# Kernel optimization log

Measured on AMD Instinct MI355X. Metric: run time of the kernel, lower is better.

The kernel has to match this reference:

```python
import jax, jax.numpy as jnp
import numpy as np

THRESHOLD = 0.05
TOP_N = 512
NMS_THR = 0.6
POST_TOP_N = 100
MIN_SIZE = 0.0
N_CLASS = 8
IMG_SIZE = (256.0, 256.0, 64.0)
B, C, H, W, D = 4, 8, 128, 128, 32


def _pairwise_iou3d(b):
    # b: [K, 6] in xyzxyz; returns [K, K] volumetric IoU
    lo, hi = b[:, :3], b[:, 3:]
    ilo = jnp.maximum(lo[:, None, :], lo[None, :, :])
    ihi = jnp.minimum(hi[:, None, :], hi[None, :, :])
    inter = jnp.prod(jnp.maximum(ihi - ilo, 0.0), axis=-1)
    vol = jnp.prod(jnp.maximum(hi - lo, 0.0), axis=-1)
    return inter / (vol[:, None] + vol[None, :] - inter + 1e-9)


def _nms_keep(boxes, scores, thr):
    # greedy NMS; scores == -1 marks invalid entries. Returns bool keep mask [K].
    K = boxes.shape[0]
    order = jnp.argsort(-scores)
    b = boxes[order]
    s = scores[order]
    iou = _pairwise_iou3d(b)
    idx = jnp.arange(K)

    def body(i, keep):
        sup = (iou[i] > thr) & keep[i] & (idx > i)
        return keep & ~sup

    keep = jax.lax.fori_loop(0, K, body, s > 0.0)
    return jnp.zeros(K, dtype=bool).at[order].set(keep)


def _forward(location, cls_pred, box_pred, center_pred):
    Bb, Cc = cls_pred.shape[0], cls_pred.shape[1]
    N = cls_pred.shape[2] * cls_pred.shape[3] * cls_pred.shape[4]
    # [B, C, H, W, D] -> [B, N, C]
    cls = jax.nn.sigmoid(cls_pred).transpose(0, 2, 3, 4, 1).reshape(Bb, N, Cc)
    ctr = jax.nn.sigmoid(center_pred).transpose(0, 2, 3, 4, 1).reshape(Bb, N)
    box = box_pred.transpose(0, 2, 3, 4, 1).reshape(Bb, N, 6)

    candid = cls > THRESHOLD                      # [B, N, C]
    scores = cls * ctr[:, :, None]                # centerness-weighted
    flat = jnp.where(candid, scores, -1.0).reshape(Bb, N * Cc)
    vals, idx = jax.lax.top_k(flat, TOP_N)        # fixed-size stand-in for mask+topk
    valid = vals > 0.0                            # matches torch clamp(count, top_n)

    loc_idx = idx // Cc                           # flattened spatial location
    class_id = idx % Cc + 1                       # labels are 1-based
    bsel = jnp.take_along_axis(box, loc_idx[..., None], axis=1)   # [B, K, 6]
    lsel = location[loc_idx]                                      # [B, K, 3]
    det = jnp.concatenate([lsel - bsel[..., :3], lsel + bsel[..., 3:]], axis=-1)

    # BoxList.clip to image volume
    full = jnp.concatenate([jnp.asarray(IMG_SIZE), jnp.asarray(IMG_SIZE)]).astype(det.dtype) - 1.0
    det = jnp.clip(det, 0.0, full)

    score = jnp.where(valid, jnp.sqrt(jnp.where(valid, vals, 1.0)), 0.0)

    # remove_small_boxes
    sides = det[..., 3:] - det[..., :3]
    valid = valid & jnp.all(sides >= MIN_SIZE, axis=-1)

    # per-class greedy NMS (decisions are non-differentiable; torch detaches anyway)
    det_ng = jax.lax.stop_gradient(det)
    score_ng = jax.lax.stop_gradient(score)

    def per_image(b_i, s_i, c_i, v_i):
        def per_class(j):
            m = v_i & (c_i == j)
            return _nms_keep(b_i, jnp.where(m, s_i, -1.0), NMS_THR) & m
        return jnp.any(jax.vmap(per_class)(jnp.arange(1, N_CLASS + 1)), axis=0)

    valid = jax.vmap(per_image)(det_ng, score_ng, class_id, valid)

    # post_top_n selection (kthvalue threshold == keep top post_top_n scores)
    fv, fi = jax.lax.top_k(jnp.where(valid, score_ng, -1.0), POST_TOP_N)
    fvalid = fv > 0.0
    fbox = jnp.take_along_axis(det, fi[..., None], axis=1) * fvalid[..., None]
    fscore = jnp.where(fvalid, jnp.take_along_axis(score, fi, axis=1), 0.0)
    flabel = jnp.where(fvalid, jnp.take_along_axis(class_id, fi, axis=1), 0)
    return fbox, fscore, flabel, fvalid


def setup_inputs() -> dict:
    key = jax.random.key(0)
    k1, k2, k3, k4 = jax.random.split(key, 4)
    N = H * W * D
    location = jax.random.uniform(k1, (N, 3), dtype=jnp.float32) * jnp.asarray(IMG_SIZE, jnp.float32)
    cls_pred = jax.random.normal(k2, (B, C, H, W, D), dtype=jnp.float32) - 2.0  # realistic logits
    box_pred = jax.random.uniform(k3, (B, 6, H, W, D), dtype=jnp.float32) * 20.0  # positive extents
    center_pred = jax.random.normal(k4, (B, 1, H, W, D), dtype=jnp.float32)
    return {"location": location, "cls_pred": cls_pred, "box_pred": box_pred, "center_pred": center_pred}


def reference(location, cls_pred, box_pred, center_pred):
    return _forward(location, cls_pred, box_pred, center_pred)
```

## Files before the change

### kernel.cpp

```cpp
#include <hip/hip_runtime.h>

#define NB 4
#define NC 8
#define NLOC 524288
#define TOPN 512
#define POST 100
#define NBIN 8192
#define SELBINS 4096
#define SCAP 4096
#define CAP 16384
#define KPT 16
#define LCAP 2048
#define NMS_THR 0.6f
#define CAND_THR 0.05f
#define SPEC_THR 0.5f

typedef unsigned long long ull;

#define OFF_CNT    0
#define OFF_OVF    16
#define OFF_KEYS   64
#define ZERO_BYTES 32

__device__ __forceinline__ float sigmoidf_(float x) {
    return 1.0f / (1.0f + __expf(-x));
}

__global__ __launch_bounds__(256) void gather_spec(const float* __restrict__ cls,
                                                   const float* __restrict__ ctr,
                                                   ull* __restrict__ keys,
                                                   unsigned int* __restrict__ counts,
                                                   unsigned int* __restrict__ ovf) {
    __shared__ ull lkeys[LCAP];
    __shared__ unsigned int lcnt;
    __shared__ unsigned int lbase;
    const int b = blockIdx.y;
    if (threadIdx.x == 0) lcnt = 0;
    __syncthreads();

    const int n0 = (blockIdx.x * blockDim.x + threadIdx.x) * 8;
    const float4* cvp = (const float4*)(ctr + (size_t)b * NLOC + n0);
    const float4 cv0 = cvp[0], cv1 = cvp[1];
    float4 cl0[NC], cl1[NC];
    #pragma unroll
    for (int c = 0; c < NC; ++c) {
        const float4* p = (const float4*)(cls + ((size_t)b * NC + c) * NLOC + n0);
        cl0[c] = p[0];
        cl1[c] = p[1];
    }

    #pragma unroll
    for (int h = 0; h < 2; ++h) {
        const float4 cv = h ? cv1 : cv0;
        #pragma unroll
        for (int j = 0; j < 4; ++j) {
            bool any = false;
            #pragma unroll
            for (int c = 0; c < NC; ++c) {
                const float x = h ? ((const float*)&cl1[c])[j] : ((const float*)&cl0[c])[j];
                any |= (x > 0.0f);
            }
            if (any) {
                const float sc = sigmoidf_(((const float*)&cv)[j]);
                #pragma unroll
                for (int c = 0; c < NC; ++c) {
                    const float x = h ? ((const float*)&cl1[c])[j] : ((const float*)&cl0[c])[j];
                    if (x > 0.0f) {
                        const float p = sigmoidf_(x) * sc;
                        if (p > SPEC_THR) {
                            const unsigned pos = atomicAdd(&lcnt, 1u);
                            if (pos < LCAP) {
                                const unsigned flat = (unsigned)((n0 + h * 4 + j) * NC + c);
                                lkeys[pos] = ((ull)__float_as_uint(p) << 32) | (unsigned)(~flat);
                            }
                        }
                    }
                }
            }
        }
    }
    __syncthreads();
    const unsigned m = lcnt;
    if (threadIdx.x == 0) {
        const unsigned stored = (m > LCAP) ? LCAP : m;
        lbase = atomicAdd(&counts[b], stored);
        if (m > LCAP) ovf[b] = 1;
    }
    __syncthreads();
    const unsigned stored = (m > LCAP) ? LCAP : m;
    const unsigned base = lbase;
    for (unsigned i = threadIdx.x; i < stored; i += blockDim.x) {
        const unsigned pos = base + i;
        if (pos < CAP) keys[(size_t)b * CAP + pos] = lkeys[i];
    }
}

__device__ __forceinline__ float iou3d_(const float* a, const float* bx) {
    const float ix = fminf(a[3], bx[3]) - fmaxf(a[0], bx[0]);
    const float iy = fminf(a[4], bx[4]) - fmaxf(a[1], bx[1]);
    const float iz = fminf(a[5], bx[5]) - fmaxf(a[2], bx[2]);
    const float inter = fmaxf(ix, 0.0f) * fmaxf(iy, 0.0f) * fmaxf(iz, 0.0f);
    const float v0 = fmaxf(a[3] - a[0], 0.0f) * fmaxf(a[4] - a[1], 0.0f) * fmaxf(a[5] - a[2], 0.0f);
    const float v1 = fmaxf(bx[3] - bx[0], 0.0f) * fmaxf(bx[4] - bx[1], 0.0f) * fmaxf(bx[5] - bx[2], 0.0f);
    return inter / (v0 + v1 - inter + 1e-9f);
}

__global__ __launch_bounds__(1024) void select_nms_kernel(const float* __restrict__ cls,
                                                          const float* __restrict__ ctr,
                                                          ull* __restrict__ keys,
                                                          unsigned int* __restrict__ counts,
                                                          const unsigned int* __restrict__ ovf,
                                                          const float* __restrict__ loc,
                                                          const float* __restrict__ box,
                                                          float* __restrict__ out) {
    __shared__ union SU {
        struct { unsigned int hist[SELBINS]; ull surv[SCAP]; } sel;
        unsigned int fhist[NBIN];
        struct { float sd[TOPN * 6]; float ss[TOPN]; int scl[TOPN];
                 int keep[TOPN]; int clist[NC][TOPN]; int wcnt[NC]; } nms;
    } u;
    __shared__ ull tk[TOPN];
    __shared__ unsigned int scnt;
    __shared__ int cut_s;

    const int b = blockIdx.x, t = threadIdx.x;

    {
        const unsigned cnt0 = counts[b];
        const bool bad = !(cnt0 >= TOPN && cnt0 <= CAP && ovf[b] == 0);
        if (bad) {
            for (int i = t; i < NBIN; i += 1024) u.fhist[i] = 0;
            __syncthreads();
            for (int n = t; n < NLOC; n += 1024) {
                const float sc = sigmoidf_(ctr[(size_t)b * NLOC + n]);
                #pragma unroll
                for (int c = 0; c < NC; ++c) {
                    const float s = sigmoidf_(cls[((size_t)b * NC + c) * NLOC + n]);
                    if (s > CAND_THR) atomicAdd(&u.fhist[__float_as_uint(s * sc) >> 17], 1u);
                }
            }
            __syncthreads();
            if (t == 0) {
                unsigned cum = 0; int bin = 0;
                for (int i = NBIN - 1; i >= 0; --i) {
                    cum += u.fhist[i];
                    if (cum >= TOPN) { bin = i; break; }
                }
                cut_s = bin;
                counts[b] = 0;
            }
            __syncthreads();
            const unsigned cb2 = (unsigned)cut_s;
            for (int n = t; n < NLOC; n += 1024) {
                const float sc = sigmoidf_(ctr[(size_t)b * NLOC + n]);
                #pragma unroll
                for (int c = 0; c < NC; ++c) {
                    const float s = sigmoidf_(cls[((size_t)b * NC + c) * NLOC + n]);
                    if (s > CAND_THR) {
                        const unsigned bits = __float_as_uint(s * sc);
                        if ((bits >> 17) >= cb2) {
                            const unsigned pos = atomicAdd(&counts[b], 1u);
                            if (pos < CAP)
                                keys[(size_t)b * CAP + pos] =
                                    ((ull)bits << 32) | (unsigned)(~(unsigned)(n * NC + c));
                        }
                    }
                }
            }
            __threadfence();
        }
    }
    __syncthreads();

    const int M = (int)min(counts[b], (unsigned)CAP);

    ull kr[KPT];
    {
        const ulonglong2* kb = (const ulonglong2*)(keys + (size_t)b * CAP);
        #pragma unroll
        for (int p = 0; p < KPT / 2; ++p) {
            const ulonglong2 v = kb[p * 1024 + t];
            kr[2 * p] = v.x;
            kr[2 * p + 1] = v.y;
        }
    }

    for (int i = t; i < SELBINS; i += 1024) u.sel.hist[i] = 0;
    if (t == 0) scnt = 0;
    if (t < TOPN) tk[t] = 0;
    __syncthreads();
    #pragma unroll
    for (int p = 0; p < KPT / 2; ++p) {
        #pragma unroll
        for (int q = 0; q < 2; ++q) {
            const int i = 2 * (p * 1024 + t) + q;
            if (i < M) {
                const unsigned hi = (unsigned)(kr[2 * p + q] >> 32);
                const int off = (int)hi - 0x3F000000;
                int bin = (off < 0) ? 0 : (off >> 11);
                if (bin > SELBINS - 1) bin = SELBINS - 1;
                atomicAdd(&u.sel.hist[bin], 1u);
            }
        }
    }
    __syncthreads();

    if (t < 64) {
        unsigned s = 0;
        for (int i = 0; i < 64; ++i)
            s += u.sel.hist[t * 64 + ((i + t) & 63)];
        unsigned suf = s;
        #pragma unroll
        for (int d = 1; d < 64; d <<= 1) {
            const unsigned o = __shfl_down(suf, d);
            suf += (t + d < 64) ? o : 0u;
        }
        const ull mask = __ballot(suf >= TOPN);
        unsigned nxt = __shfl_down(suf, 1);
        if (t == 63) nxt = 0;
        if (mask == 0ull) {
            if (t == 0) cut_s = 0;
        } else {
            const int L = 63 - __builtin_clzll(mask);
            if (t == L) {
                unsigned cum = nxt;
                int c = L * 64;
                for (int i = 63; i >= 0; --i) {
                    cum += u.sel.hist[L * 64 + i];
                    if (cum >= TOPN) { c = L * 64 + i; break; }
                }
                cut_s = c;
            }
        }
    }
    __syncthreads();

    const int cb = cut_s;
    #pragma unroll
    for (int p = 0; p < KPT / 2; ++p) {
        #pragma unroll
        for (int q = 0; q < 2; ++q) {
            const int i = 2 * (p * 1024 + t) + q;
            if (i < M) {
                const ull k = kr[2 * p + q];
                const unsigned hi = (unsigned)(k >> 32);
                const int off = (int)hi - 0x3F000000;
                int bin = (off < 0) ? 0 : (off >> 11);
                if (bin > SELBINS - 1) bin = SELBINS - 1;
                if (bin >= cb) {
                    const unsigned p2 = atomicAdd(&scnt, 1u);
                    if (p2 < SCAP) u.sel.surv[p2] = k;
                }
            }
        }
    }
    __syncthreads();

    const unsigned sc_final = scnt;
    if (sc_final <= (unsigned)SCAP) {
        const int S = (int)sc_final;
        for (int i = t; i < S; i += 1024) {
            const ull ke = u.sel.surv[i];
            int r = 0;
            for (int j = 0; j < S; ++j) r += (u.sel.surv[j] > ke) ? 1 : 0;
            if (r < TOPN) tk[r] = ke;
        }
    } else {
        for (int i = t; i < M; i += 1024) {
            const ull ke = keys[(size_t)b * CAP + i];
            int r = 0;
            for (int j = 0; j < M; ++j) r += (keys[(size_t)b * CAP + j] > ke) ? 1 : 0;
            if (r < TOPN) tk[r] = ke;
        }
    }
    __syncthreads();

    if (t < TOPN) {
        const ull k = tk[t];
        const unsigned bits = (unsigned)(k >> 32);
        const float val = __uint_as_float(bits);
        int valid = (val > 0.0f) ? 1 : 0;
        const unsigned flat = ~(unsigned)(k & 0xffffffffu);
        int n = 0, c = 0;
        if (valid) { n = (int)(flat >> 3); c = (int)(flat & 7u); }
        const float lx = loc[n * 3 + 0], ly = loc[n * 3 + 1], lz = loc[n * 3 + 2];
        const float* bp = box + (size_t)b * 6 * NLOC + n;
        const float b0 = bp[0];
        const float b1 = bp[(size_t)NLOC];
        const float b2 = bp[2 * (size_t)NLOC];
        const float b3 = bp[3 * (size_t)NLOC];
        const float b4 = bp[4 * (size_t)NLOC];
        const float b5 = bp[5 * (size_t)NLOC];
        const float d0 = fminf(fmaxf(lx - b0, 0.0f), 255.0f);
        const float d1 = fminf(fmaxf(ly - b1, 0.0f), 255.0f);
        const float d2 = fminf(fmaxf(lz - b2, 0.0f), 63.0f);
        const float d3 = fminf(fmaxf(lx + b3, 0.0f), 255.0f);
        const float d4 = fminf(fmaxf(ly + b4, 0.0f), 255.0f);
        const float d5 = fminf(fmaxf(lz + b5, 0.0f), 63.0f);
        if (d3 - d0 < 0.0f || d4 - d1 < 0.0f || d5 - d2 < 0.0f) valid = 0;
        u.nms.sd[t * 6 + 0] = d0; u.nms.sd[t * 6 + 1] = d1; u.nms.sd[t * 6 + 2] = d2;
        u.nms.sd[t * 6 + 3] = d3; u.nms.sd[t * 6 + 4] = d4; u.nms.sd[t * 6 + 5] = d5;
        u.nms.ss[t] = (val > 0.0f) ? sqrtf(val) : 0.0f;
        u.nms.scl[t] = c + 1;
        u.nms.keep[t] = valid;
    }
    __syncthreads();

    if (t < TOPN) {
        const int w = t >> 6, lane = t & 63;
        const int myclass = w + 1;
        int cnt = 0;
        for (int j0 = 0; j0 < TOPN; j0 += 64) {
            const int j = j0 + lane;
            const bool pred = (u.nms.scl[j] == myclass) && (u.nms.keep[j] != 0);
            const ull m = __ballot(pred);
            if (pred) {
                const int pos = cnt + __popcll(m & ((1ull << lane) - 1ull));
                u.nms.clist[w][pos] = j;
            }
            cnt += __popcll(m);
        }
        __threadfence_block();

        if (cnt <= 128) {
            const int g0 = (lane < cnt) ? u.nms.clist[w][lane] : -1;
            const int g1 = (lane + 64 < cnt) ? u.nms.clist[w][lane + 64] : -1;
            float B0[6], B1[6];
            #pragma unroll
            for (int q = 0; q < 6; ++q) {
                B0[q] = (g0 >= 0) ? u.nms.sd[g0 * 6 + q] : 0.0f;
                B1[q] = (g1 >= 0) ? u.nms.sd[g1 * 6 + q] : 0.0f;
            }
            bool a0 = (g0 >= 0), a1 = (g1 >= 0);
            ull m0 = __ballot(a0), m1 = __ballot(a1);
            for (int i = 0; i < cnt; ++i) {
                const int ki = i >> 6, li = i & 63;
                const ull mi = ki ? m1 : m0;
                if (!((mi >> li) & 1ull)) continue;
                float pb[6];
                #pragma unroll
                for (int q = 0; q < 6; ++q) pb[q] = __shfl(ki ? B1[q] : B0[q], li);
                if (a0 && lane > i)      { if (iou3d_(B0, pb) > NMS_THR) a0 = false; }
                if (a1 && lane + 64 > i) { if (iou3d_(B1, pb) > NMS_THR) a1 = false; }
                m0 = __ballot(a0); m1 = __ballot(a1);
            }
            if (g0 >= 0 && !a0) u.nms.keep[g0] = 0;
            if (g1 >= 0 && !a1) u.nms.keep[g1] = 0;
        } else {
            volatile int* vkeep = u.nms.keep;
            const float* sd = u.nms.sd;
            for (int i = 0; i < cnt; ++i) {
                const int gi = u.nms.clist[w][i];
                if (!vkeep[gi]) continue;
                float pb[6];
                #pragma unroll
                for (int q = 0; q < 6; ++q) pb[q] = sd[gi * 6 + q];
                for (int e = i + 1 + lane; e < cnt; e += 64) {
                    const int gj = u.nms.clist[w][e];
                    if (vkeep[gj]) {
                        float cb_[6];
                        #pragma unroll
                        for (int q = 0; q < 6; ++q) cb_[q] = sd[gj * 6 + q];
                        if (iou3d_(cb_, pb) > NMS_THR) vkeep[gj] = 0;
                    }
                }
                __threadfence_block();
            }
        }
    }
    __syncthreads();

    if (t < TOPN) {
        const int w = t >> 6, lane = t & 63;
        const ull km = __ballot(u.nms.keep[t] != 0);
        if (lane == 0) u.nms.wcnt[w] = __popcll(km);
    }
    __syncthreads();
    if (t < TOPN) {
        const int w = t >> 6, lane = t & 63;
        const ull km = __ballot(u.nms.keep[t] != 0);
        int before = 0, total = 0;
        #pragma unroll
        for (int w2 = 0; w2 < NC; ++w2) {
            total += u.nms.wcnt[w2];
            if (w2 < w) before += u.nms.wcnt[w2];
        }
        const int myrank = before + __popcll(km & ((1ull << lane) - 1ull));

        float* fbox = out;
        float* fscore = out + NB * POST * 6;
        float* flabel = out + NB * POST * 7;
        float* fvalid = out + NB * POST * 8;

        if (u.nms.keep[t] && myrank < POST) {
            #pragma unroll
            for (int k = 0; k < 6; ++k) fbox[(b * POST + myrank) * 6 + k] = u.nms.sd[t * 6 + k];
            fscore[b * POST + myrank] = u.nms.ss[t];
            flabel[b * POST + myrank] = (float)u.nms.scl[t];
            fvalid[b * POST + myrank] = 1.0f;
        }
        const int tc = (total < POST) ? total : POST;
        if (t >= tc && t < POST) {
            #pragma unroll
            for (int k = 0; k < 6; ++k) fbox[(b * POST + t) * 6 + k] = 0.0f;
            fscore[b * POST + t] = 0.0f;
            flabel[b * POST + t] = 0.0f;
            fvalid[b * POST + t] = 0.0f;
        }
    }
}

extern "C" void kernel_launch(void* const* d_in, const int* in_sizes, int n_in,
                              void* d_out, int out_size, void* d_ws, size_t ws_size,
                              hipStream_t stream) {
    const float* location = (const float*)d_in[0];
    const float* cls_pred = (const float*)d_in[1];
    const float* box_pred = (const float*)d_in[2];
    const float* ctr_pred = (const float*)d_in[3];

    char* ws = (char*)d_ws;
    unsigned int* counts = (unsigned int*)(ws + OFF_CNT);
    unsigned int* ovf    = (unsigned int*)(ws + OFF_OVF);
    ull*          keys   = (ull*)(ws + OFF_KEYS);

    hipMemsetAsync(d_ws, 0, ZERO_BYTES, stream);

    gather_spec<<<dim3(NLOC / 2048, NB), 256, 0, stream>>>(cls_pred, ctr_pred, keys, counts, ovf);
    select_nms_kernel<<<NB, 1024, 0, stream>>>(cls_pred, ctr_pred, keys, counts, ovf,
                                               location, box_pred, (float*)d_out);
}
```

Baseline: 85.96 us.

## Split select/NMS into separate kernels and precompute IoU suppression bitmasks

The monolithic select+NMS kernel is split into three kernels: top-k selection writing to a global buffer, a decode kernel spread over more blocks to gather boxes, and an NMS/output kernel. Within NMS, pairwise IoU suppression bits are computed up front into per-lane bitmasks, so the serial greedy loop only does bit tests and ballots instead of shuffles and IoU math. Key loads are also guarded by count, and the rank-count loops are unrolled. This adds two kernel launches, a larger memset, and global round-trips through workspace.

```diff
diff --git a/kernel.cpp b/kernel.cpp
--- a/kernel.cpp
+++ b/kernel.cpp
@@ -19,8 +19,13 @@
 
 #define OFF_CNT    0
 #define OFF_OVF    16
-#define OFF_KEYS   64
-#define ZERO_BYTES 32
+#define OFF_TOPK   64
+#define OFF_DET    16448
+#define OFF_SS     65600
+#define OFF_SCL    73792
+#define OFF_KEEP   81984
+#define OFF_KEYS   90176
+#define ZERO_BYTES 16448
 
 __device__ __forceinline__ float sigmoidf_(float x) {
     return 1.0f / (1.0f + __expf(-x));
@@ -105,21 +110,16 @@
     return inter / (v0 + v1 - inter + 1e-9f);
 }
 
-__global__ __launch_bounds__(1024) void select_nms_kernel(const float* __restrict__ cls,
-                                                          const float* __restrict__ ctr,
-                                                          ull* __restrict__ keys,
-                                                          unsigned int* __restrict__ counts,
-                                                          const unsigned int* __restrict__ ovf,
-                                                          const float* __restrict__ loc,
-                                                          const float* __restrict__ box,
-                                                          float* __restrict__ out) {
+__global__ __launch_bounds__(1024) void select_kernel(const float* __restrict__ cls,
+                                                      const float* __restrict__ ctr,
+                                                      ull* __restrict__ keys,
+                                                      unsigned int* __restrict__ counts,
+                                                      const unsigned int* __restrict__ ovf,
+                                                      ull* __restrict__ tk_g) {
     __shared__ union SU {
         struct { unsigned int hist[SELBINS]; ull surv[SCAP]; } sel;
         unsigned int fhist[NBIN];
-        struct { float sd[TOPN * 6]; float ss[TOPN]; int scl[TOPN];
-                 int keep[TOPN]; int clist[NC][TOPN]; int wcnt[NC]; } nms;
     } u;
-    __shared__ ull tk[TOPN];
     __shared__ unsigned int scnt;
     __shared__ int cut_s;
 
@@ -179,7 +179,9 @@
         const ulonglong2* kb = (const ulonglong2*)(keys + (size_t)b * CAP);
         #pragma unroll
         for (int p = 0; p < KPT / 2; ++p) {
-            const ulonglong2 v = kb[p * 1024 + t];
+            const int vi = p * 1024 + t;
+            ulonglong2 v; v.x = 0; v.y = 0;
+            if (2 * vi < M) v = kb[vi];
             kr[2 * p] = v.x;
             kr[2 * p + 1] = v.y;
         }
@@ -187,7 +189,6 @@
 
     for (int i = t; i < SELBINS; i += 1024) u.sel.hist[i] = 0;
     if (t == 0) scnt = 0;
-    if (t < TOPN) tk[t] = 0;
     __syncthreads();
     #pragma unroll
     for (int p = 0; p < KPT / 2; ++p) {
@@ -207,6 +208,7 @@
 
     if (t < 64) {
         unsigned s = 0;
+        #pragma unroll 8
         for (int i = 0; i < 64; ++i)
             s += u.sel.hist[t * 64 + ((i + t) & 63)];
         unsigned suf = s;
@@ -262,141 +264,181 @@
         for (int i = t; i < S; i += 1024) {
             const ull ke = u.sel.surv[i];
             int r = 0;
-            for (int j = 0; j < S; ++j) r += (u.sel.surv[j] > ke) ? 1 : 0;
-            if (r < TOPN) tk[r] = ke;
+            int j = 0;
+            for (; j + 16 <= S; j += 16) {
+                #pragma unroll
+                for (int q = 0; q < 16; ++q) r += (u.sel.surv[j + q] > ke) ? 1 : 0;
+            }
+            for (; j < S; ++j) r += (u.sel.surv[j] > ke) ? 1 : 0;
+            if (r < TOPN) tk_g[b * TOPN + r] = ke;
         }
     } else {
         for (int i = t; i < M; i += 1024) {
             const ull ke = keys[(size_t)b * CAP + i];
             int r = 0;
             for (int j = 0; j < M; ++j) r += (keys[(size_t)b * CAP + j] > ke) ? 1 : 0;
-            if (r < TOPN) tk[r] = ke;
-        }
-    }
-    __syncthreads();
-
-    if (t < TOPN) {
-        const ull k = tk[t];
-        const unsigned bits = (unsigned)(k >> 32);
-        const float val = __uint_as_float(bits);
-        int valid = (val > 0.0f) ? 1 : 0;
-        const unsigned flat = ~(unsigned)(k & 0xffffffffu);
-        int n = 0, c = 0;
-        if (valid) { n = (int)(flat >> 3); c = (int)(flat & 7u); }
-        const float lx = loc[n * 3 + 0], ly = loc[n * 3 + 1], lz = loc[n * 3 + 2];
-        const float* bp = box + (size_t)b * 6 * NLOC + n;
-        const float b0 = bp[0];
-        const float b1 = bp[(size_t)NLOC];
-        const float b2 = bp[2 * (size_t)NLOC];
-        const float b3 = bp[3 * (size_t)NLOC];
-        const float b4 = bp[4 * (size_t)NLOC];
-        const float b5 = bp[5 * (size_t)NLOC];
-        const float d0 = fminf(fmaxf(lx - b0, 0.0f), 255.0f);
-        const float d1 = fminf(fmaxf(ly - b1, 0.0f), 255.0f);
-        const float d2 = fminf(fmaxf(lz - b2, 0.0f), 63.0f);
-        const float d3 = fminf(fmaxf(lx + b3, 0.0f), 255.0f);
-        const float d4 = fminf(fmaxf(ly + b4, 0.0f), 255.0f);
-        const float d5 = fminf(fmaxf(lz + b5, 0.0f), 63.0f);
-        if (d3 - d0 < 0.0f || d4 - d1 < 0.0f || d5 - d2 < 0.0f) valid = 0;
-        u.nms.sd[t * 6 + 0] = d0; u.nms.sd[t * 6 + 1] = d1; u.nms.sd[t * 6 + 2] = d2;
-        u.nms.sd[t * 6 + 3] = d3; u.nms.sd[t * 6 + 4] = d4; u.nms.sd[t * 6 + 5] = d5;
-        u.nms.ss[t] = (val > 0.0f) ? sqrtf(val) : 0.0f;
-        u.nms.scl[t] = c + 1;
-        u.nms.keep[t] = valid;
-    }
-    __syncthreads();
-
-    if (t < TOPN) {
-        const int w = t >> 6, lane = t & 63;
-        const int myclass = w + 1;
-        int cnt = 0;
-        for (int j0 = 0; j0 < TOPN; j0 += 64) {
-            const int j = j0 + lane;
-            const bool pred = (u.nms.scl[j] == myclass) && (u.nms.keep[j] != 0);
-            const ull m = __ballot(pred);
-            if (pred) {
-                const int pos = cnt + __popcll(m & ((1ull << lane) - 1ull));
-                u.nms.clist[w][pos] = j;
-            }
-            cnt += __popcll(m);
-        }
-        __threadfence_block();
-
-        if (cnt <= 128) {
-            const int g0 = (lane < cnt) ? u.nms.clist[w][lane] : -1;
-            const int g1 = (lane + 64 < cnt) ? u.nms.clist[w][lane + 64] : -1;
-            float B0[6], B1[6];
+            if (r < TOPN) tk_g[b * TOPN + r] = ke;
+        }
+    }
+}
+
+__global__ __launch_bounds__(64) void decode_kernel(const ull* __restrict__ tk_g,
+                                                    const float* __restrict__ loc,
+                                                    const float* __restrict__ box,
+                                                    float* __restrict__ det,
+                                                    float* __restrict__ ss,
+                                                    int* __restrict__ scl,
+                                                    int* __restrict__ keepo) {
+    const int b = blockIdx.y;
+    const int t = blockIdx.x * 64 + threadIdx.x;
+    const ull k = tk_g[b * TOPN + t];
+    const unsigned bits = (unsigned)(k >> 32);
+    const float val = __uint_as_float(bits);
+    int valid = (val > 0.0f) ? 1 : 0;
+    const unsigned flat = ~(unsigned)(k & 0xffffffffu);
+    int n = 0, c = 0;
+    if (valid) { n = (int)(flat >> 3); c = (int)(flat & 7u); }
+    const float lx = loc[n * 3 + 0], ly = loc[n * 3 + 1], lz = loc[n * 3 + 2];
+    const float* bp = box + (size_t)b * 6 * NLOC + n;
+    const float b0 = bp[0];
+    const float b1 = bp[(size_t)NLOC];
+    const float b2 = bp[2 * (size_t)NLOC];
+    const float b3 = bp[3 * (size_t)NLOC];
+    const float b4 = bp[4 * (size_t)NLOC];
+    const float b5 = bp[5 * (size_t)NLOC];
+    const float d0 = fminf(fmaxf(lx - b0, 0.0f), 255.0f);
+    const float d1 = fminf(fmaxf(ly - b1, 0.0f), 255.0f);
+    const float d2 = fminf(fmaxf(lz - b2, 0.0f), 63.0f);
+    const float d3 = fminf(fmaxf(lx + b3, 0.0f), 255.0f);
+    const float d4 = fminf(fmaxf(ly + b4, 0.0f), 255.0f);
+    const float d5 = fminf(fmaxf(lz + b5, 0.0f), 63.0f);
+    if (d3 - d0 < 0.0f || d4 - d1 < 0.0f || d5 - d2 < 0.0f) valid = 0;
+    const int o = b * TOPN + t;
+    det[o * 6 + 0] = d0; det[o * 6 + 1] = d1; det[o * 6 + 2] = d2;
+    det[o * 6 + 3] = d3; det[o * 6 + 4] = d4; det[o * 6 + 5] = d5;
+    ss[o] = (val > 0.0f) ? sqrtf(val) : 0.0f;
+    scl[o] = c + 1;
+    keepo[o] = valid;
+}
+
+__global__ __launch_bounds__(512) void nms_out_kernel(const float* __restrict__ det,
+                                                      const float* __restrict__ score,
+                                                      const int* __restrict__ clsid,
+                                                      const int* __restrict__ validin,
+                                                      float* __restrict__ out) {
+    __shared__ float sd[TOPN * 6];
+    __shared__ float ss[TOPN];
+    __shared__ int scl[TOPN];
+    __shared__ int keep[TOPN];
+    __shared__ int clist[NC][TOPN];
+    __shared__ int wcnt[NC];
+    const int b = blockIdx.x, t = threadIdx.x;
+    const int w = t >> 6, lane = t & 63;
+
+    {
+        const float* dp = det + (size_t)(b * TOPN) * 6;
+        for (int i = t; i < TOPN * 6; i += 512) sd[i] = dp[i];
+    }
+    ss[t] = score[b * TOPN + t];
+    scl[t] = clsid[b * TOPN + t];
+    keep[t] = validin[b * TOPN + t];
+    __syncthreads();
+
+    const int myclass = w + 1;
+    int cnt = 0;
+    for (int j0 = 0; j0 < TOPN; j0 += 64) {
+        const int j = j0 + lane;
+        const bool pred = (scl[j] == myclass) && (keep[j] != 0);
+        const ull m = __ballot(pred);
+        if (pred) {
+            const int pos = cnt + __popcll(m & ((1ull << lane) - 1ull));
+            clist[w][pos] = j;
+        }
+        cnt += __popcll(m);
+    }
+    __threadfence_block();
+
+    if (cnt <= 128) {
+        const int g0 = (lane < cnt) ? clist[w][lane] : -1;
+        const int g1 = (lane + 64 < cnt) ? clist[w][lane + 64] : -1;
+        float A0[6], A1[6];
+        #pragma unroll
+        for (int q = 0; q < 6; ++q) {
+            A0[q] = (g0 >= 0) ? sd[g0 * 6 + q] : 0.0f;
+            A1[q] = (g1 >= 0) ? sd[g1 * 6 + q] : 0.0f;
+        }
+        ull s0 = 0, s1lo = 0, s1hi = 0;
+        for (int i = 0; i < cnt; ++i) {
+            const int gi = clist[w][i];
+            float pb[6];
             #pragma unroll
-            for (int q = 0; q < 6; ++q) {
-                B0[q] = (g0 >= 0) ? u.nms.sd[g0 * 6 + q] : 0.0f;
-                B1[q] = (g1 >= 0) ? u.nms.sd[g1 * 6 + q] : 0.0f;
-            }
-            bool a0 = (g0 >= 0), a1 = (g1 >= 0);
-            ull m0 = __ballot(a0), m1 = __ballot(a1);
-            for (int i = 0; i < cnt; ++i) {
-                const int ki = i >> 6, li = i & 63;
-                const ull mi = ki ? m1 : m0;
-                if (!((mi >> li) & 1ull)) continue;
-                float pb[6];
-                #pragma unroll
-                for (int q = 0; q < 6; ++q) pb[q] = __shfl(ki ? B1[q] : B0[q], li);
-                if (a0 && lane > i)      { if (iou3d_(B0, pb) > NMS_THR) a0 = false; }
-                if (a1 && lane + 64 > i) { if (iou3d_(B1, pb) > NMS_THR) a1 = false; }
-                m0 = __ballot(a0); m1 = __ballot(a1);
-            }
-            if (g0 >= 0 && !a0) u.nms.keep[g0] = 0;
-            if (g1 >= 0 && !a1) u.nms.keep[g1] = 0;
-        } else {
-            volatile int* vkeep = u.nms.keep;
-            const float* sd = u.nms.sd;
-            for (int i = 0; i < cnt; ++i) {
-                const int gi = u.nms.clist[w][i];
-                if (!vkeep[gi]) continue;
-                float pb[6];
-                #pragma unroll
-                for (int q = 0; q < 6; ++q) pb[q] = sd[gi * 6 + q];
-                for (int e = i + 1 + lane; e < cnt; e += 64) {
-                    const int gj = u.nms.clist[w][e];
-                    if (vkeep[gj]) {
-                        float cb_[6];
-                        #pragma unroll
-                        for (int q = 0; q < 6; ++q) cb_[q] = sd[gj * 6 + q];
-                        if (iou3d_(cb_, pb) > NMS_THR) vkeep[gj] = 0;
-                    }
-                }
-                __threadfence_block();
-            }
-        }
-    }
-    __syncthreads();
-
-    if (t < TOPN) {
-        const int w = t >> 6, lane = t & 63;
-        const ull km = __ballot(u.nms.keep[t] != 0);
-        if (lane == 0) u.nms.wcnt[w] = __popcll(km);
-    }
-    __syncthreads();
-    if (t < TOPN) {
-        const int w = t >> 6, lane = t & 63;
-        const ull km = __ballot(u.nms.keep[t] != 0);
+            for (int q = 0; q < 6; ++q) pb[q] = sd[gi * 6 + q];
+            if (i < 64) {
+                if (g0 >= 0 && lane > i && iou3d_(A0, pb) > NMS_THR) s0 |= 1ull << i;
+                if (g1 >= 0 && iou3d_(A1, pb) > NMS_THR) s1lo |= 1ull << i;
+            } else {
+                if (g1 >= 0 && (i - 64) < lane && iou3d_(A1, pb) > NMS_THR) s1hi |= 1ull << (i - 64);
+            }
+        }
+        bool a0 = (g0 >= 0), a1 = (g1 >= 0);
+        ull m0 = __ballot(a0), m1 = __ballot(a1);
+        for (int i = 0; i < cnt; ++i) {
+            const bool alive_i = (i < 64) ? ((m0 >> i) & 1ull) : ((m1 >> (i - 64)) & 1ull);
+            if (!alive_i) continue;
+            if (a0 && i < 64 && ((s0 >> i) & 1ull)) a0 = false;
+            if (a1) {
+                const bool sb = (i < 64) ? ((s1lo >> i) & 1ull) : ((s1hi >> (i - 64)) & 1ull);
+                if (sb) a1 = false;
+            }
+            m0 = __ballot(a0); m1 = __ballot(a1);
+        }
+        if (g0 >= 0 && !a0) keep[g0] = 0;
+        if (g1 >= 0 && !a1) keep[g1] = 0;
+    } else {
+        volatile int* vkeep = keep;
+        for (int i = 0; i < cnt; ++i) {
+            const int gi = clist[w][i];
+            if (!vkeep[gi]) continue;
+            float pb[6];
+            #pragma unroll
+            for (int q = 0; q < 6; ++q) pb[q] = sd[gi * 6 + q];
+            for (int e = i + 1 + lane; e < cnt; e += 64) {
+                const int gj = clist[w][e];
+                if (vkeep[gj]) {
+                    float cb_[6];
+                    #pragma unroll
+                    for (int q = 0; q < 6; ++q) cb_[q] = sd[gj * 6 + q];
+                    if (iou3d_(cb_, pb) > NMS_THR) vkeep[gj] = 0;
+                }
+            }
+            __threadfence_block();
+        }
+    }
+    __syncthreads();
+
+    const ull km = __ballot(keep[t] != 0);
+    if (lane == 0) wcnt[w] = __popcll(km);
+    __syncthreads();
+    {
+        const ull km2 = __ballot(keep[t] != 0);
         int before = 0, total = 0;
         #pragma unroll
         for (int w2 = 0; w2 < NC; ++w2) {
-            total += u.nms.wcnt[w2];
-            if (w2 < w) before += u.nms.wcnt[w2];
-        }
-        const int myrank = before + __popcll(km & ((1ull << lane) - 1ull));
+            total += wcnt[w2];
+            if (w2 < w) before += wcnt[w2];
+        }
+        const int myrank = before + __popcll(km2 & ((1ull << lane) - 1ull));
 
         float* fbox = out;
         float* fscore = out + NB * POST * 6;
         float* flabel = out + NB * POST * 7;
         float* fvalid = out + NB * POST * 8;
 
-        if (u.nms.keep[t] && myrank < POST) {
+        if (keep[t] && myrank < POST) {
             #pragma unroll
-            for (int k = 0; k < 6; ++k) fbox[(b * POST + myrank) * 6 + k] = u.nms.sd[t * 6 + k];
-            fscore[b * POST + myrank] = u.nms.ss[t];
-            flabel[b * POST + myrank] = (float)u.nms.scl[t];
+            for (int k = 0; k < 6; ++k) fbox[(b * POST + myrank) * 6 + k] = sd[t * 6 + k];
+            fscore[b * POST + myrank] = ss[t];
+            flabel[b * POST + myrank] = (float)scl[t];
             fvalid[b * POST + myrank] = 1.0f;
         }
         const int tc = (total < POST) ? total : POST;
@@ -421,11 +463,17 @@
     char* ws = (char*)d_ws;
     unsigned int* counts = (unsigned int*)(ws + OFF_CNT);
     unsigned int* ovf    = (unsigned int*)(ws + OFF_OVF);
+    ull*          tk     = (ull*)(ws + OFF_TOPK);
+    float*        det    = (float*)(ws + OFF_DET);
+    float*        ss     = (float*)(ws + OFF_SS);
+    int*          scl    = (int*)(ws + OFF_SCL);
+    int*          keep   = (int*)(ws + OFF_KEEP);
     ull*          keys   = (ull*)(ws + OFF_KEYS);
 
     hipMemsetAsync(d_ws, 0, ZERO_BYTES, stream);
 
     gather_spec<<<dim3(NLOC / 2048, NB), 256, 0, stream>>>(cls_pred, ctr_pred, keys, counts, ovf);
-    select_nms_kernel<<<NB, 1024, 0, stream>>>(cls_pred, ctr_pred, keys, counts, ovf,
-                                               location, box_pred, (float*)d_out);
-}
+    select_kernel<<<NB, 1024, 0, stream>>>(cls_pred, ctr_pred, keys, counts, ovf, tk);
+    decode_kernel<<<dim3(8, NB), 64, 0, stream>>>(tk, location, box_pred, det, ss, scl, keep);
+    nms_out_kernel<<<NB, 512, 0, stream>>>(det, ss, scl, keep, (float*)d_out);
+}
```

Measured after the change: 90.07 us. 4.8% more time.
